# Optimization experiments

Measured on AMD Instinct MI355X. Metric: run time of the kernel, lower is better.

Reference implementation:

```python
import jax, jax.numpy as jnp
import numpy as np

NHID, NHEAD, HEAD_DIM, AL = 256, 10, 10, 2


def conv1x1(t, w, b):
    # t: [B, Cin, H, W], w: [Cout, Cin], b: [Cout]  (1x1 Conv2d)
    return jnp.einsum('bchw,oc->bohw', t, w) + b[None, :, None, None]


def setup_inputs() -> dict:
    key = jax.random.key(0)
    ks = jax.random.split(key, 12)
    B, L = 4, 2048
    d = NHEAD * HEAD_DIM  # 100
    sc_in = 1.0 / np.sqrt(NHID)
    sc_att = 1.0 / np.sqrt(3 * d)
    return {
        'x': jax.random.normal(ks[0], (B, NHID, L, 1), jnp.float32),
        'ax': jax.random.normal(ks[1], (B, NHID, AL, L), jnp.float32),
        'edge_matrix': jax.random.uniform(ks[2], (B, L, L), jnp.float32),
        'wq': jax.random.normal(ks[3], (d, NHID), jnp.float32) * sc_in,
        'bq': jnp.zeros((d,), jnp.float32),
        'wk': jax.random.normal(ks[4], (d, NHID), jnp.float32) * sc_in,
        'bk': jnp.zeros((d,), jnp.float32),
        'wv': jax.random.normal(ks[5], (d, NHID), jnp.float32) * sc_in,
        'bv': jnp.zeros((d,), jnp.float32),
        'wo': jax.random.normal(ks[6], (NHID, 3 * d), jnp.float32) * sc_att,
        'bo': jnp.zeros((NHID,), jnp.float32),
    }


def reference(x, ax, edge_matrix, wq, bq, wk, bk, wv, bv, wo, bo):
    B, _, L, _ = x.shape
    nh, hd = NHEAD, HEAD_DIM
    # NOTE: original torch code overwrites k and v with q (k=q.view, v=q.view),
    # so WK(x)/WV(x) are dead code; WK/WV are only applied to ax.
    q = conv1x1(x, wq, bq).reshape(B, nh, hd, 1, L)          # [B,nh,hd,1,L]
    ak = conv1x1(ax, wk, bk).reshape(B, nh, hd, AL, L)       # [B,nh,hd,aL,L]
    av = conv1x1(ax, wv, bv).reshape(B, nh, hd, AL, L)
    k = jnp.concatenate([q, ak], axis=3)                      # [B,nh,hd,1+aL,L]
    v = jnp.concatenate([q, av], axis=3)
    D = hd * (1 + AL)                                         # 30
    k = k.reshape(B, nh, D, L).transpose(0, 1, 3, 2)          # [B,nh,L,D]
    v = v.reshape(B, nh, D, L).transpose(0, 1, 3, 2)
    scores = jnp.einsum('bhld,bhmd->bhlm', k, v)              # [B,nh,L,L]
    alpha = jax.nn.softmax(scores * edge_matrix[:, None] / np.sqrt(hd), axis=-1)
    # dropout in eval mode (identity)
    att = jnp.einsum('bhlm,bhmd->bhld', alpha, v)             # [B,nh,L,D]
    # torch .view(B,-1,L,1) is a raw row-major reshape of the (B*nh,L,D) buffer
    att = att.reshape(B, nh * D, L, 1)
    return conv1x1(att, wo, bo)                               # [B,nhid,L,1]
```

## Files before the change

kernel.cpp:

```cpp
#include <hip/hip_runtime.h>
#include <hip/hip_bf16.h>
#include <math.h>

#define L 2048
#define NH 10
#define DP 32
#define D30 30

typedef __attribute__((ext_vector_type(8))) short bf16x8;
typedef __attribute__((ext_vector_type(4))) float f32x4;

__device__ inline short f2bf(float f) {
    union { float f; unsigned u; } v; v.f = f;
    unsigned r = (v.u + 0x7FFF + ((v.u >> 16) & 1)) >> 16;
    return (short)r;
}
__device__ inline unsigned pk2(float a, float b) {
    unsigned ua = __float_as_uint(a) + 0x8000u;
    unsigned ub = __float_as_uint(b) + 0x8000u;
    return (ua >> 16) | (ub & 0xFFFF0000u);
}
__device__ inline int permL(int l) {
    return (l & ~63) | ((l & 15) << 2) | ((l >> 4) & 3);
}

#define GLD16(g, l) __builtin_amdgcn_global_load_lds( \
    (__attribute__((address_space(1))) void*)(g),     \
    (__attribute__((address_space(3))) void*)(l), 16, 0, 0)

__global__ __launch_bounds__(256) void proj_kernel(
    const float* __restrict__ x, const float* __restrict__ ax,
    const float* __restrict__ wq, const float* __restrict__ bq,
    const float* __restrict__ wk, const float* __restrict__ bk,
    const float* __restrict__ wv, const float* __restrict__ bv,
    const float* __restrict__ wo, short* __restrict__ wo16,
    short* __restrict__ Kbuf, short* __restrict__ Vbuf, short* __restrict__ Vtbuf)
{
    const int t  = threadIdx.x;
    const int og = blockIdx.y;
    const int b  = blockIdx.z;

    if (og == 5) {
        int id = (b * 32 + blockIdx.x) * 256 + t;
        if (id < 20480) {
            int idx = id * 4;
            int o = idx / 320, c = idx % 320;
            float v0 = (c + 0 < 300) ? wo[o * 300 + c + 0] : 0.f;
            float v1 = (c + 1 < 300) ? wo[o * 300 + c + 1] : 0.f;
            float v2 = (c + 2 < 300) ? wo[o * 300 + c + 2] : 0.f;
            float v3 = (c + 3 < 300) ? wo[o * 300 + c + 3] : 0.f;
            uint2 u; u.x = pk2(v0, v1); u.y = pk2(v2, v3);
            *(uint2*)&wo16[idx] = u;
        }
        return;
    }

    __shared__ __align__(16) short Wl[112 * 72];
    __shared__ __align__(16) short XT[64 * 72];
    const int l0 = blockIdx.x * 64;

    const float* W; const float* bias;
    if (og == 0)      { W = wq; bias = bq; }
    else if (og <= 2) { W = wk; bias = bk; }
    else              { W = wv; bias = bv; }
    const int al = (og - 1) & 1;

    const int wid  = t >> 6;
    const int lane = t & 63;
    const int quad = lane >> 4;
    const int l15  = lane & 15;

    f32x4 acc[7];
    #pragma unroll
    for (int ot = 0; ot < 7; ot++) acc[ot] = (f32x4){0,0,0,0};

    const int cq = (t & 15) * 4;
    const int lq = (t >> 4) * 4;
    const size_t rs = (og == 0) ? (size_t)L : (size_t)(2 * L);

    for (int cc = 0; cc < 4; cc++) {
        const int c0 = cc * 64;
        __syncthreads();
        #pragma unroll
        for (int it = 0; it < 7; it++) {
            int kk = (t + it * 256) * 4;
            int o = kk >> 6, c = kk & 63;
            f32x4 v = {0, 0, 0, 0};
            if (o < 100) v = *(const f32x4*)(W + (size_t)o * 256 + c0 + c);
            uint2 u; u.x = pk2(v[0], v[1]); u.y = pk2(v[2], v[3]);
            *(uint2*)&Wl[o * 72 + c] = u;
        }
        {
            const float* src = (og == 0)
                ? x  + ((size_t)(b * 256 + c0 + cq)) * L + l0 + lq
                : ax + (((size_t)(b * 256 + c0 + cq)) * 2 + al) * L + l0 + lq;
            f32x4 r0 = *(const f32x4*)(src);
            f32x4 r1 = *(const f32x4*)(src + rs);
            f32x4 r2 = *(const f32x4*)(src + 2 * rs);
            f32x4 r3 = *(const f32x4*)(src + 3 * rs);
            #pragma unroll
            for (int i = 0; i < 4; i++) {
                uint2 u; u.x = pk2(r0[i], r1[i]); u.y = pk2(r2[i], r3[i]);
                *(uint2*)&XT[(lq + i) * 72 + cq] = u;
            }
        }
        __syncthreads();
        #pragma unroll
        for (int ks = 0; ks < 2; ks++) {
            bf16x8 bfrag = *(const bf16x8*)&XT[(wid * 16 + l15) * 72 + ks * 32 + quad * 8];
            #pragma unroll
            for (int ot = 0; ot < 7; ot++) {
                bf16x8 afrag = *(const bf16x8*)&Wl[(ot * 16 + l15) * 72 + ks * 32 + quad * 8];
                acc[ot] = __builtin_amdgcn_mfma_f32_16x16x32_bf16(afrag, bfrag, acc[ot], 0, 0, 0);
            }
        }
    }

    const int part = (og == 0) ? 0 : ((og == 1 || og == 3) ? 1 : 2);
    const float KS = 0.31622776601683794f * 1.4426950408889634f;
    const int l = l0 + wid * 16 + l15;
    #pragma unroll
    for (int ot = 0; ot < 7; ot++) {
        #pragma unroll
        for (int r = 0; r < 4; r++) {
            int o = ot * 16 + quad * 4 + r;
            if (o >= 100) continue;
            float val = acc[ot][r] + bias[o];
            int h = o / 10, dd = 3 * (o % 10) + part;
            size_t rowb = ((size_t)(b * NH + h)) * L;
            size_t tb   = ((size_t)(b * NH + h) * DP + dd) * L;
            if (og == 0) {
                Kbuf[(rowb + l) * DP + dd] = f2bf(val * KS);
                short s = f2bf(val);
                Vbuf[(rowb + l) * DP + dd] = s;
                Vtbuf[tb + permL(l)] = s;
            } else if (og <= 2) {
                Kbuf[(rowb + l) * DP + dd] = f2bf(val * KS);
            } else {
                short s = f2bf(val);
                Vbuf[(rowb + l) * DP + dd] = s;
                Vtbuf[tb + permL(l)] = s;
            }
        }
    }
}

__global__ __launch_bounds__(256, 5) void attn_kernel(
    const short* __restrict__ K, const short* __restrict__ V,
    const short* __restrict__ Vt, const float* __restrict__ edge,
    float* __restrict__ Opart, float* __restrict__ lsums, int npart)
{
    __shared__ __align__(16) short Vl[2][64 * 32];
    __shared__ __align__(16) short Vtl[2][32 * 64];
    __shared__ __align__(16) short Pm[4][16 * 72];
    const int t    = threadIdx.x;
    const int wid  = t >> 6;
    const int lane = t & 63;
    const int quad = lane >> 4;
    const int l15  = lane & 15;

    const int id  = blockIdx.x;
    const int gg  = id / 40;
    const int rem = id - gg * 40;
    const int h2  = rem >> 3;
    const int g   = gg * 8 + (rem & 7);
    const int lb  = g & 31;
    const int b   = (g >> 5) & 3;
    const int mz  = g >> 7;

    const int l0 = lb * 64;
    const int h0 = h2 * 2;
    const size_t bh0 = (size_t)(b * NH + h0), bh1 = bh0 + 1;
    const int mbase = mz * (L / npart);
    const int nit   = (L / npart) / 64;

    const int lrow = l0 + wid * 16 + l15;
    bf16x8 kf[2];
    kf[0] = *(const bf16x8*)(K + (bh0 * L + lrow) * DP + quad * 8);
    kf[1] = *(const bf16x8*)(K + (bh1 * L + lrow) * DP + quad * 8);

    const int myrow = l0 + wid * 16 + quad * 4;
    const float* ep[4];
    #pragma unroll
    for (int r = 0; r < 4; r++)
        ep[r] = edge + (size_t)b * L * L + (size_t)(myrow + r) * L + l15 + mbase;

    const int sh = wid & 1;
    const size_t sbh = bh0 + sh;
    const short* sgp;
    if (wid < 2)
        sgp = V + (sbh * L + mbase + (lane >> 2)) * DP + (((lane & 3) ^ ((lane >> 3) & 3)) * 8);
    else
        sgp = Vt + (sbh * DP + (lane >> 3)) * L + mbase + (((lane & 7) ^ ((lane >> 3) & 7)) * 8);

    float ls[2][4] = {{0,0,0,0},{0,0,0,0}};
    f32x4 O[2][2] = {{{0,0,0,0},{0,0,0,0}},{{0,0,0,0},{0,0,0,0}}};
    const f32x4 z = {0,0,0,0};

    for (int mt = 0; mt < nit; mt++) {
        __syncthreads();
        if (wid < 2) {
            #pragma unroll
            for (int k = 0; k < 4; k++)
                GLD16(sgp + k * (16 * DP), &Vl[sh][k * 512]);
        } else {
            #pragma unroll
            for (int k = 0; k < 4; k++)
                GLD16(sgp + (size_t)k * (8 * L), &Vtl[sh][k * 512]);
        }
        float e[4][4];
        #pragma unroll
        for (int r = 0; r < 4; r++)
            #pragma unroll
            for (int nb = 0; nb < 4; nb++)
                e[nb][r] = ep[r][nb * 16];
        __syncthreads();

        short* P = &Pm[wid][0];
        #pragma unroll
        for (int hh = 0; hh < 2; hh++) {
            f32x4 S[4];
            #pragma unroll
            for (int nb = 0; nb < 4; nb++) {
                int sw = (quad ^ ((l15 >> 1) & 3)) * 8;
                bf16x8 vf = *(const bf16x8*)&Vl[hh][(nb * 16 + l15) * 32 + sw];
                S[nb] = __builtin_amdgcn_mfma_f32_16x16x32_bf16(kf[hh], vf, z, 0, 0, 0);
            }
            #pragma unroll
            for (int r = 0; r < 4; r++) {
                float p0 = __builtin_amdgcn_exp2f(S[0][r] * e[0][r]);
                float p1 = __builtin_amdgcn_exp2f(S[1][r] * e[1][r]);
                float p2 = __builtin_amdgcn_exp2f(S[2][r] * e[2][r]);
                float p3 = __builtin_amdgcn_exp2f(S[3][r] * e[3][r]);
                ls[hh][r] += (p0 + p1) + (p2 + p3);
                uint2 u; u.x = pk2(p0, p1); u.y = pk2(p2, p3);
                *(uint2*)&P[(quad * 4 + r) * 72 + l15 * 4] = u;
            }
            #pragma unroll
            for (int ks = 0; ks < 2; ks++) {
                int go = ((ks * 4 + quad) ^ (l15 & 7)) * 8;
                bf16x8 a  = *(const bf16x8*)&P[l15 * 72 + ks * 32 + quad * 8];
                bf16x8 b0 = *(const bf16x8*)&Vtl[hh][l15 * 64 + go];
                bf16x8 b1 = *(const bf16x8*)&Vtl[hh][(16 + l15) * 64 + go];
                O[hh][0] = __builtin_amdgcn_mfma_f32_16x16x32_bf16(a, b0, O[hh][0], 0, 0, 0);
                O[hh][1] = __builtin_amdgcn_mfma_f32_16x16x32_bf16(a, b1, O[hh][1], 0, 0, 0);
            }
        }
        #pragma unroll
        for (int r = 0; r < 4; r++) ep[r] += 64;
        sgp += (wid < 2) ? 64 * DP : 64;
    }

    float* ab  = Opart + (size_t)mz * 2457600 + (size_t)b * 614400;
    float* lsp = lsums + (size_t)mz * 81920 + (size_t)b * 20480;
    #pragma unroll
    for (int r = 0; r < 4; r++) {
        float s0 = ls[0][r];
        s0 += __shfl_xor(s0, 1); s0 += __shfl_xor(s0, 2);
        s0 += __shfl_xor(s0, 4); s0 += __shfl_xor(s0, 8);
        float s1 = ls[1][r];
        s1 += __shfl_xor(s1, 1); s1 += __shfl_xor(s1, 2);
        s1 += __shfl_xor(s1, 4); s1 += __shfl_xor(s1, 8);
        int lr = myrow + r;
        if (l15 == 0) {
            lsp[h0 * L + lr]       = s0;
            lsp[(h0 + 1) * L + lr] = s1;
        }
        size_t base0 = (size_t)h0 * 61440 + (size_t)lr * D30;
        ab[base0 + l15]         = O[0][0][r];
        ab[base0 + 61440 + l15] = O[1][0][r];
        if (l15 < 14) {
            ab[base0 + 16 + l15]         = O[0][1][r];
            ab[base0 + 61440 + 16 + l15] = O[1][1][r];
        }
    }
}

__global__ __launch_bounds__(256, 4) void out_kernel(
    const float* __restrict__ Opart, const float* __restrict__ lsums,
    const short* __restrict__ wo16, const float* __restrict__ bo,
    float* __restrict__ out, int npart)
{
    __shared__ __align__(16) short XT[32 * 72];
    const int t    = threadIdx.x;
    const int wid  = t >> 6;
    const int lane = t & 63;
    const int quad = lane >> 4;
    const int l15  = lane & 15;
    const int m0 = blockIdx.x * 32;
    const int o0 = blockIdx.y * 64;
    const int b  = blockIdx.z;
    const float* P0b = Opart + (size_t)b * 614400;
    const float* P1b = Opart + 2457600 + (size_t)b * 614400;
    const float* ls0 = lsums + (size_t)b * 20480;
    const float* ls1 = lsums + 81920 + (size_t)b * 20480;

    f32x4 acc0 = {0,0,0,0}, acc1 = {0,0,0,0};
    const int cb = t >> 4;
    const int mb = t & 15;
    const short* wrow = wo16 + (size_t)(o0 + wid * 16 + l15) * 320;

    for (int cc = 0; cc < 5; cc++) {
        const int c0 = cc * 64;
        __syncthreads();
        {
            int crb = c0 + cb * 4;
            float vx[4], vy[4];
            #pragma unroll
            for (int i = 0; i < 4; i++) {
                int cr = crb + i; if (cr > 299) cr = 299;
                int f = cr * 2048 + m0 + mb * 2;
                float2 p = *(const float2*)(P0b + f);
                int j0 = f / 30, j1 = (f + 1) / 30;
                float s0 = ls0[j0], s1 = ls0[j1];
                if (npart == 2) {
                    float2 q = *(const float2*)(P1b + f);
                    p.x += q.x; p.y += q.y;
                    s0 += ls1[j0]; s1 += ls1[j1];
                }
                vx[i] = p.x * __builtin_amdgcn_rcpf(s0);
                vy[i] = p.y * __builtin_amdgcn_rcpf(s1);
            }
            uint2 u0; u0.x = pk2(vx[0], vx[1]); u0.y = pk2(vx[2], vx[3]);
            *(uint2*)&XT[(mb * 2 + 0) * 72 + cb * 4] = u0;
            uint2 u1; u1.x = pk2(vy[0], vy[1]); u1.y = pk2(vy[2], vy[3]);
            *(uint2*)&XT[(mb * 2 + 1) * 72 + cb * 4] = u1;
        }
        __syncthreads();
        #pragma unroll
        for (int ks = 0; ks < 2; ks++) {
            bf16x8 a  = *(const bf16x8*)(wrow + c0 + ks * 32 + quad * 8);
            bf16x8 b0 = *(const bf16x8*)&XT[l15 * 72 + ks * 32 + quad * 8];
            bf16x8 b1 = *(const bf16x8*)&XT[(16 + l15) * 72 + ks * 32 + quad * 8];
            acc0 = __builtin_amdgcn_mfma_f32_16x16x32_bf16(a, b0, acc0, 0, 0, 0);
            acc1 = __builtin_amdgcn_mfma_f32_16x16x32_bf16(a, b1, acc1, 0, 0, 0);
        }
    }
    #pragma unroll
    for (int r = 0; r < 4; r++) {
        int o = o0 + wid * 16 + quad * 4 + r;
        float bb = bo[o];
        float* orow = out + ((size_t)(b * 256 + o)) * L;
        orow[m0 + l15]      = acc0[r] + bb;
        orow[m0 + 16 + l15] = acc1[r] + bb;
    }
}

extern "C" void kernel_launch(void* const* d_in, const int* in_sizes, int n_in,
                              void* d_out, int out_size, void* d_ws, size_t ws_size,
                              hipStream_t stream) {
    const float* x    = (const float*)d_in[0];
    const float* ax   = (const float*)d_in[1];
    const float* edge = (const float*)d_in[2];
    const float* wq   = (const float*)d_in[3];
    const float* bq   = (const float*)d_in[4];
    const float* wk   = (const float*)d_in[5];
    const float* bk   = (const float*)d_in[6];
    const float* wv   = (const float*)d_in[7];
    const float* bv   = (const float*)d_in[8];
    const float* wo   = (const float*)d_in[9];
    const float* bo   = (const float*)d_in[10];
    float* out = (float*)d_out;

    const size_t KB  = (size_t)4 * NH * L * DP * 2;
    const size_t PSZ = (size_t)2457600 * 4;
    const size_t LSZ = (size_t)81920 * 4;
    const size_t WOS = (size_t)256 * 320 * 2;
    char* ws = (char*)d_ws;
    short* Kbuf  = (short*)ws;
    short* Vbuf  = (short*)(ws + KB);
    short* Vtbuf = (short*)(ws + 2 * KB);
    float* P0    = (float*)(ws + 3 * KB);
    int npart = (ws_size >= 3 * KB + 2 * PSZ + 2 * LSZ + WOS) ? 2 : 1;
    float* lsums = (float*)(ws + 3 * KB + (size_t)npart * PSZ);
    short* wo16  = (short*)(ws + 3 * KB + (size_t)npart * (PSZ + LSZ));
    if (ws_size < 3 * KB + PSZ + LSZ + WOS) return;

    hipMemsetAsync(ws, 0, 3 * KB, stream);

    proj_kernel<<<dim3(32, 6, 4), 256, 0, stream>>>(x, ax, wq, bq, wk, bk, wv, bv,
                                                    wo, wo16, Kbuf, Vbuf, Vtbuf);
    attn_kernel<<<dim3(640 * npart), 256, 0, stream>>>(Kbuf, Vbuf, Vtbuf, edge,
                                                       P0, lsums, npart);
    out_kernel<<<dim3(64, 4, 4), 256, 0, stream>>>(P0, lsums, wo16, bo, out, npart);
}
```

Before: 221.1 us.

## Fold softmax row sums into PV MFMA via ones column; use hardware bf16 pack

Writes a column of bf16 ones into padding column 30 of the transposed V buffer, so the P·V MFMA also produces the softmax row sum in output column 30. This removes the per-element sum accumulation and the shuffle reductions. The bf16 packing helper now uses the hardware cvt_pk_bf16_f32 builtin when it is available. The x/ax tile load in the projection kernel is also restructured into coalesced scalar loads along L. The row sum now comes from bf16-rounded P values, and it relies on proj_kernel writing the ones column, which is ordered only by kernel launch order.

Result: no change. 225.0 us (+1.8%).

```diff
diff --git a/kernel.cpp b/kernel.cpp
--- a/kernel.cpp
+++ b/kernel.cpp
@@ -15,10 +15,17 @@
     unsigned r = (v.u + 0x7FFF + ((v.u >> 16) & 1)) >> 16;
     return (short)r;
 }
-__device__ inline unsigned pk2(float a, float b) {
+__device__ inline unsigned pkbf(float a, float b) {
+#if __has_builtin(__builtin_amdgcn_cvt_pk_bf16_f32)
+    typedef __attribute__((ext_vector_type(2))) __bf16 bf2;
+    union { bf2 v; unsigned u; } x;
+    x.v = __builtin_amdgcn_cvt_pk_bf16_f32(a, b);
+    return x.u;
+#else
     unsigned ua = __float_as_uint(a) + 0x8000u;
     unsigned ub = __float_as_uint(b) + 0x8000u;
     return (ua >> 16) | (ub & 0xFFFF0000u);
+#endif
 }
 __device__ inline int permL(int l) {
     return (l & ~63) | ((l & 15) << 2) | ((l >> 4) & 3);
@@ -49,8 +56,12 @@
             float v1 = (c + 1 < 300) ? wo[o * 300 + c + 1] : 0.f;
             float v2 = (c + 2 < 300) ? wo[o * 300 + c + 2] : 0.f;
             float v3 = (c + 3 < 300) ? wo[o * 300 + c + 3] : 0.f;
-            uint2 u; u.x = pk2(v0, v1); u.y = pk2(v2, v3);
+            uint2 u; u.x = pkbf(v0, v1); u.y = pkbf(v2, v3);
             *(uint2*)&wo16[idx] = u;
+            int j = id * 4;
+            int bh = j >> 11, l = j & 2047;
+            uint2 one; one.x = 0x3F803F80u; one.y = 0x3F803F80u;
+            *(uint2*)&Vtbuf[((size_t)bh * DP + 30) * L + l] = one;
         }
         return;
     }
@@ -74,9 +85,12 @@
     #pragma unroll
     for (int ot = 0; ot < 7; ot++) acc[ot] = (f32x4){0,0,0,0};
 
-    const int cq = (t & 15) * 4;
-    const int lq = (t >> 4) * 4;
-    const size_t rs = (og == 0) ? (size_t)L : (size_t)(2 * L);
+    const int rs = (og == 0) ? L : (2 * L);
+    const float* srcb = (og == 0)
+        ? x  + (size_t)(b * 256) * L
+        : ax + ((size_t)(b * 256) * 2 + al) * L;
+    const int lx = t & 31;
+    const int px = t >> 5;
 
     for (int cc = 0; cc < 4; cc++) {
         const int c0 = cc * 64;
@@ -87,22 +101,17 @@
             int o = kk >> 6, c = kk & 63;
             f32x4 v = {0, 0, 0, 0};
             if (o < 100) v = *(const f32x4*)(W + (size_t)o * 256 + c0 + c);
-            uint2 u; u.x = pk2(v[0], v[1]); u.y = pk2(v[2], v[3]);
+            uint2 u; u.x = pkbf(v[0], v[1]); u.y = pkbf(v[2], v[3]);
             *(uint2*)&Wl[o * 72 + c] = u;
         }
-        {
-            const float* src = (og == 0)
-                ? x  + ((size_t)(b * 256 + c0 + cq)) * L + l0 + lq
-                : ax + (((size_t)(b * 256 + c0 + cq)) * 2 + al) * L + l0 + lq;
-            f32x4 r0 = *(const f32x4*)(src);
-            f32x4 r1 = *(const f32x4*)(src + rs);
-            f32x4 r2 = *(const f32x4*)(src + 2 * rs);
-            f32x4 r3 = *(const f32x4*)(src + 3 * rs);
-            #pragma unroll
-            for (int i = 0; i < 4; i++) {
-                uint2 u; u.x = pk2(r0[i], r1[i]); u.y = pk2(r2[i], r3[i]);
-                *(uint2*)&XT[(lq + i) * 72 + cq] = u;
-            }
+        #pragma unroll
+        for (int ps = 0; ps < 4; ps++) {
+            int c = (ps * 8 + px) * 2;
+            const float* s = srcb + (size_t)(c0 + c) * rs + l0;
+            float a0 = s[lx],      a1 = s[rs + lx];
+            float b0 = s[lx + 32], b1 = s[rs + lx + 32];
+            *(unsigned*)&XT[lx * 72 + c]        = pkbf(a0, a1);
+            *(unsigned*)&XT[(lx + 32) * 72 + c] = pkbf(b0, b1);
         }
         __syncthreads();
         #pragma unroll
@@ -193,7 +202,6 @@
     else
         sgp = Vt + (sbh * DP + (lane >> 3)) * L + mbase + (((lane & 7) ^ ((lane >> 3) & 7)) * 8);
 
-    float ls[2][4] = {{0,0,0,0},{0,0,0,0}};
     f32x4 O[2][2] = {{{0,0,0,0},{0,0,0,0}},{{0,0,0,0},{0,0,0,0}}};
     const f32x4 z = {0,0,0,0};
 
@@ -232,8 +240,7 @@
                 float p1 = __builtin_amdgcn_exp2f(S[1][r] * e[1][r]);
                 float p2 = __builtin_amdgcn_exp2f(S[2][r] * e[2][r]);
                 float p3 = __builtin_amdgcn_exp2f(S[3][r] * e[3][r]);
-                ls[hh][r] += (p0 + p1) + (p2 + p3);
-                uint2 u; u.x = pk2(p0, p1); u.y = pk2(p2, p3);
+                uint2 u; u.x = pkbf(p0, p1); u.y = pkbf(p2, p3);
                 *(uint2*)&P[(quad * 4 + r) * 72 + l15 * 4] = u;
             }
             #pragma unroll
@@ -252,26 +259,20 @@
     }
 
     float* ab  = Opart + (size_t)mz * 2457600 + (size_t)b * 614400;
-    float* lsp = lsums + (size_t)mz * 81920 + (size_t)b * 20480;
+    float* lsp = lsums + (size_t)mz * 81920  + (size_t)b * 20480;
     #pragma unroll
     for (int r = 0; r < 4; r++) {
-        float s0 = ls[0][r];
-        s0 += __shfl_xor(s0, 1); s0 += __shfl_xor(s0, 2);
-        s0 += __shfl_xor(s0, 4); s0 += __shfl_xor(s0, 8);
-        float s1 = ls[1][r];
-        s1 += __shfl_xor(s1, 1); s1 += __shfl_xor(s1, 2);
-        s1 += __shfl_xor(s1, 4); s1 += __shfl_xor(s1, 8);
         int lr = myrow + r;
-        if (l15 == 0) {
-            lsp[h0 * L + lr]       = s0;
-            lsp[(h0 + 1) * L + lr] = s1;
-        }
-        size_t base0 = (size_t)h0 * 61440 + (size_t)lr * D30;
+        size_t base0 = (size_t)h0 * 61440 + (size_t)lr * 30;
         ab[base0 + l15]         = O[0][0][r];
         ab[base0 + 61440 + l15] = O[1][0][r];
         if (l15 < 14) {
             ab[base0 + 16 + l15]         = O[0][1][r];
             ab[base0 + 61440 + 16 + l15] = O[1][1][r];
+        }
+        if (l15 == 14) {
+            lsp[h0 * L + lr]       = O[0][1][r];
+            lsp[(h0 + 1) * L + lr] = O[1][1][r];
         }
     }
 }
@@ -321,9 +322,9 @@
                 vx[i] = p.x * __builtin_amdgcn_rcpf(s0);
                 vy[i] = p.y * __builtin_amdgcn_rcpf(s1);
             }
-            uint2 u0; u0.x = pk2(vx[0], vx[1]); u0.y = pk2(vx[2], vx[3]);
+            uint2 u0; u0.x = pkbf(vx[0], vx[1]); u0.y = pkbf(vx[2], vx[3]);
             *(uint2*)&XT[(mb * 2 + 0) * 72 + cb * 4] = u0;
-            uint2 u1; u1.x = pk2(vy[0], vy[1]); u1.y = pk2(vy[2], vy[3]);
+            uint2 u1; u1.x = pkbf(vy[0], vy[1]); u1.y = pkbf(vy[2], vy[3]);
             *(uint2*)&XT[(mb * 2 + 1) * 72 + cb * 4] = u1;
         }
         __syncthreads();
```
